# Kernel tuning notes

Measured on AMD Instinct MI355X. Metric: run time of the kernel, lower is better.

## Reference

```python
import jax, jax.numpy as jnp
import numpy as np

SCALE = 2
PAD = 4
EPS = 1e-5
K = 5
N, C, H, W = 4, 64, 128, 128


def _splits(a, s):
    # (..., W, H) -> (..., W/s, H/s, s*s), block decimation matching torch view/permute
    *lead, Wd, Hd = a.shape
    b = a.reshape(*lead, s, Wd // s, s, Hd // s)
    nl = len(lead)
    b = jnp.transpose(b, tuple(range(nl)) + (nl + 1, nl + 3, nl, nl + 2))
    return b.reshape(*lead, Wd // s, Hd // s, s * s)


def _p2o(psf, Hs, Ws):
    # PSF -> OTF: zero-pad, roll to center at origin, FFT
    kh, kw = psf.shape[-2], psf.shape[-1]
    otf = jnp.zeros(psf.shape[:-2] + (Hs, Ws), psf.dtype).at[..., :kh, :kw].set(psf)
    otf = jnp.roll(otf, (-(kh // 2), -(kw // 2)), axis=(-2, -1))
    return jnp.fft.fftn(otf, axes=(-2, -1))


def _upsample(x, s):
    # s-fold zero-filling upsampler (S^T y)
    n, c, h, w = x.shape
    return jnp.zeros((n, c, h * s, w * s), x.dtype).at[..., ::s, ::s].set(x)


def setup_inputs() -> dict:
    key = jax.random.key(0)
    kx, kw_, _ = jax.random.split(key, 3)
    x = jax.random.normal(kx, (N, C, H, W), dtype=jnp.float32)
    w_raw = jax.random.normal(kw_, (1, C, K, K), dtype=jnp.float32)
    weight = jax.nn.softmax(w_raw.reshape(1, C, -1), axis=-1).reshape(1, C, K, K)
    bias = jnp.zeros((1, C, 1, 1), dtype=jnp.float32)
    return {"x": x, "weight": weight, "bias": bias}


def reference(x, weight, bias):
    s = SCALE
    xp = jnp.pad(x, ((0, 0), (0, 0), (PAD, PAD), (PAD, PAD)), mode="wrap")  # circular
    biaseps = jax.nn.sigmoid(bias - 9.0) + EPS  # (1,C,1,1)
    _, _, h, w = xp.shape
    STy = _upsample(xp, s)  # zero-filled upsample
    # nearest-neighbor interpolate by integer factor s
    xn = jnp.repeat(jnp.repeat(xp, s, axis=-2), s, axis=-1)
    FB = _p2o(weight, h * s, w * s)           # (1,C,hs,ws) complex
    FBC = jnp.conj(FB)
    F2B = jnp.abs(FB) ** 2                     # real
    FBFy = FBC * jnp.fft.fftn(STy, axes=(-2, -1))
    FR = FBFy + jnp.fft.fftn(biaseps * xn, axes=(-2, -1))
    x1 = FB * FR
    FBR = jnp.mean(_splits(x1, s), axis=-1)    # (N,C,h,w) complex
    invW = jnp.mean(_splits(F2B, s), axis=-1)  # (1,C,h,w) real
    invWBR = FBR / (invW + biaseps)
    FCBinvWBR = FBC * jnp.tile(invWBR, (1, 1, s, s))
    FX = (FR - FCBinvWBR) / biaseps
    out = jnp.real(jnp.fft.ifftn(FX, axes=(-2, -1)))
    out = out[..., PAD * s:-PAD * s, PAD * s:-PAD * s]
    return out
```

## Files before the change

### kernel.cpp

```cpp
#include <hip/hip_runtime.h>
#include <math.h>


#define MDIM 136
#define RSC  70
#define HC   69
#define PLANE_HALF (MDIM*HC)
#define NPLANES 256
#define LDS_CPLX (MDIM*RSC + MDIM)
#define PI_D 3.14159265358979323846
#define NTH 1024

__device__ __forceinline__ int slot136(int k) { return 17*(k & 7) + (k >> 3); }
__device__ __forceinline__ int slot68(int k)  { return 17*(k & 3) + (k >> 2); }

template<int DIR, class F>
__device__ __forceinline__ void dft17_sink(float2* z, int base, int stride, F f)
{
    constexpr float C17[9] = {1.f, 0.93247223f, 0.73900892f, 0.44573836f,
                              0.09226836f, -0.27366299f, -0.60263464f,
                              -0.85021714f, -0.98297310f};
    constexpr float S17[9] = {0.f, 0.36124167f, 0.67369564f, 0.89516329f,
                              0.99573418f, 0.96182564f, 0.79801723f,
                              0.52643216f, 0.18374952f};
    constexpr float d = (DIR > 0) ? 1.f : -1.f;
    float xr[17], xi[17];
#pragma unroll
    for (int n = 0; n < 17; n++) {
        float2 v = z[base + n*stride];
        xr[n] = v.x; xi[n] = v.y;
    }
    float ar[8], ai[8], br[8], bi[8];
#pragma unroll
    for (int n = 1; n <= 8; n++) {
        ar[n-1] = xr[n] + xr[17-n];  ai[n-1] = xi[n] + xi[17-n];
        br[n-1] = xr[n] - xr[17-n];  bi[n-1] = xi[n] - xi[17-n];
    }
    float s0r = xr[0], s0i = xi[0];
#pragma unroll
    for (int n = 0; n < 8; n++) { s0r += ar[n]; s0i += ai[n]; }
    f(0, s0r, s0i);
#pragma unroll
    for (int k = 1; k <= 8; k++) {
        float Pr = xr[0], Pi = xi[0], Qr = 0.f, Qi = 0.f;
#pragma unroll
        for (int n = 1; n <= 8; n++) {
            int m = (k*n) % 17;
            float cc = (m <= 8) ? C17[m] : C17[17-m];
            float ss = (m <= 8) ? S17[m] : -S17[17-m];
            Pr = fmaf(ar[n-1], cc, Pr);
            Pi = fmaf(ai[n-1], cc, Pi);
            Qr = fmaf(br[n-1], ss, Qr);
            Qi = fmaf(bi[n-1], ss, Qi);
        }
        f(k,    Pr - d*Qi, Pi + d*Qr);
        f(17-k, Pr + d*Qi, Pi - d*Qr);
    }
}

template<int DIR>
__device__ __forceinline__ void radix4_tw(float2* z, const float2* lut, int base, int n2,
                                          float2 Z0, float2 Z1, float2 Z2, float2 Z3)
{
    constexpr float d = (DIR > 0) ? 1.0f : -1.0f;
    float t0r = Z0.x+Z2.x, t0i = Z0.y+Z2.y;
    float t1r = Z0.x-Z2.x, t1i = Z0.y-Z2.y;
    float t2r = Z1.x+Z3.x, t2i = Z1.y+Z3.y;
    float t3r = Z1.x-Z3.x, t3i = Z1.y-Z3.y;
    float X0r = t0r+t2r,     X0i = t0i+t2i;
    float X2r = t0r-t2r,     X2i = t0i-t2i;
    float X1r = t1r - d*t3i, X1i = t1i + d*t3r;
    float X3r = t1r + d*t3i, X3i = t1i - d*t3r;
    z[base + n2] = make_float2(X0r, X0i);
    float2 w1 = lut[2*n2], w2 = lut[4*n2], w3 = lut[6*n2];
    z[base + 17 + n2] = make_float2(X1r*w1.x - X1i*w1.y, X1r*w1.y + X1i*w1.x);
    z[base + 34 + n2] = make_float2(X2r*w2.x - X2i*w2.y, X2r*w2.y + X2i*w2.x);
    z[base + 51 + n2] = make_float2(X3r*w3.x - X3i*w3.y, X3r*w3.y + X3i*w3.x);
}

template<int DIR>
__device__ void fft136_s1(float2* z, const float2* lut, int ncols, int tid)
{
    constexpr float d = (DIR > 0) ? 1.0f : -1.0f;
    constexpr float C707 = 0.70710678118654752f;
    int c = tid / 17;
    int n2 = tid - c*17;
    for (int e = tid; e < ncols*17; e += NTH) {
        float xr[8], xi[8];
#pragma unroll
        for (int n1 = 0; n1 < 8; n1++) {
            float2 v = z[(17*n1 + n2)*RSC + c];
            xr[n1] = v.x; xi[n1] = v.y;
        }
        float e0r = xr[0]+xr[4], e0i = xi[0]+xi[4];
        float e1r = xr[0]-xr[4], e1i = xi[0]-xi[4];
        float o0r = xr[2]+xr[6], o0i = xi[2]+xi[6];
        float o1r = xr[2]-xr[6], o1i = xi[2]-xi[6];
        float E0r = e0r+o0r, E0i = e0i+o0i;
        float E2r = e0r-o0r, E2i = e0i-o0i;
        float E1r = e1r - d*o1i, E1i = e1i + d*o1r;
        float E3r = e1r + d*o1i, E3i = e1i - d*o1r;
        float f0r = xr[1]+xr[5], f0i = xi[1]+xi[5];
        float f1r = xr[1]-xr[5], f1i = xi[1]-xi[5];
        float h0r = xr[3]+xr[7], h0i = xi[3]+xi[7];
        float h1r = xr[3]-xr[7], h1i = xi[3]-xi[7];
        float O0r = f0r+h0r, O0i = f0i+h0i;
        float O2r = f0r-h0r, O2i = f0i-h0i;
        float O1r = f1r - d*h1i, O1i = f1i + d*h1r;
        float O3r = f1r + d*h1i, O3i = f1i - d*h1r;
        float t1r =  C707*(O1r - d*O1i), t1i = C707*(O1i + d*O1r);
        float t2r = -d*O2i,              t2i = d*O2r;
        float t3r = -C707*(O3r + d*O3i), t3i = C707*(d*O3r - O3i);
        float Xr[8], Xi[8];
        Xr[0]=E0r+O0r; Xi[0]=E0i+O0i;  Xr[4]=E0r-O0r; Xi[4]=E0i-O0i;
        Xr[1]=E1r+t1r; Xi[1]=E1i+t1i;  Xr[5]=E1r-t1r; Xi[5]=E1i-t1i;
        Xr[2]=E2r+t2r; Xi[2]=E2i+t2i;  Xr[6]=E2r-t2r; Xi[6]=E2i-t2i;
        Xr[3]=E3r+t3r; Xi[3]=E3i+t3i;  Xr[7]=E3r-t3r; Xi[7]=E3i-t3i;
        z[n2*RSC + c] = make_float2(Xr[0], Xi[0]);
        int ti = 0;
#pragma unroll
        for (int k1 = 1; k1 < 8; k1++) {
            ti += n2;
            float2 w = lut[ti];
            z[(17*k1 + n2)*RSC + c] = make_float2(Xr[k1]*w.x - Xi[k1]*w.y,
                                                  Xr[k1]*w.y + Xi[k1]*w.x);
        }
        c += 60; n2 += 4; if (n2 >= 17) { n2 -= 17; c++; }
    }
}

template<int DIR>
__device__ void ct68_s1(float2* z, const float2* lut, int tid)
{
    int row = tid / 17;
    int n2  = tid - row*17;
    for (int e = tid; e < MDIM*17; e += NTH) {
        int base = row*RSC;
        float2 Z0 = z[base + n2];
        float2 Z1 = z[base + 17 + n2];
        float2 Z2 = z[base + 34 + n2];
        float2 Z3 = z[base + 51 + n2];
        radix4_tw<DIR>(z, lut, base, n2, Z0, Z1, Z2, Z3);
        row += 60; n2 += 4; if (n2 >= 17) { n2 -= 17; row++; }
    }
}

__device__ __forceinline__ float2 c2r_pack(float2 a, float2 b, float2 w)
{
    float Sr = a.x + b.x, Si = a.y - b.y;
    float Dr = a.x - b.x, Di = a.y + b.y;
    float Or = w.x*Dr - w.y*Di, Oi = w.x*Di + w.y*Dr;
    return make_float2(Sr - Oi, Si + Or);
}

__global__ __launch_bounds__(1024, 8) void fwd_kernel(const float* __restrict__ x,
                                                      float2* __restrict__ Xhat)
{
    extern __shared__ float2 zsm[];
    float2* z   = zsm;
    float2* lut = zsm + MDIM*RSC;
    const int tid = threadIdx.x;

    if (tid < MDIM) {
        float s, c; sincosf(-2.0f*(float)PI_D*(float)tid/136.0f, &s, &c);
        lut[tid] = make_float2(c, s);
    }
    const float* xp = x + (size_t)blockIdx.x * (128*128);
    {
        int i = tid / 68, n = tid - (tid/68)*68;
        for (int e = tid; e < MDIM*68; e += NTH) {
            int si = (i + 124) & 127;
            int j0 = (2*n + 124) & 127;
            z[i*RSC + n] = *reinterpret_cast<const float2*>(xp + si*128 + j0);
            i += 15; n += 4; if (n >= 68) { n -= 68; i++; }
        }
    }
    __syncthreads();
    ct68_s1<-1>(z, lut, tid);
    __syncthreads();
    if (tid < MDIM*4) {
        int row = tid >> 2, k1 = tid & 3;
        int base = row*RSC + 17*k1;
        dft17_sink<-1>(z, base, 1, [&](int k2, float re, float im) {
            z[base + k2] = make_float2(re, im);
        });
    }
    __syncthreads();
    {
        int row = tid / 35, k = tid - (tid/35)*35;
        for (int e = tid; e < MDIM*35; e += NTH) {
            int base = row*RSC;
            int sa = slot68(k);
            float2 Za = z[base+sa];
            float Zar = Za.x, Zai = Za.y;
            float Zbr, Zbi; int sb;
            if (k == 0) { Zbr = Zar; Zbi = Zai; sb = 68; }
            else {
                int kk = 68-k; sb = slot68(kk);
                float2 Zb = z[base+sb]; Zbr = Zb.x; Zbi = Zb.y;
            }
            float2 w = lut[k];
            float wc = w.x, ws = w.y;
            float Er = 0.5f*(Zar + Zbr), Ei = 0.5f*(Zai - Zbi);
            float Dr = 0.5f*(Zar - Zbr), Di = 0.5f*(Zai + Zbi);
            float Tr = wc*Dr - ws*Di, Ti = wc*Di + ws*Dr;
            z[base+sa] = make_float2(Er + Ti, Ei - Tr);
            float E2r = Er,  E2i = -Ei;
            float D2r = -Dr, D2i = Di;
            float w2c = -wc, w2s = ws;
            float T2r = w2c*D2r - w2s*D2i, T2i = w2c*D2i + w2s*D2r;
            z[base+sb] = make_float2(E2r + T2i, E2i - T2r);
            row += 29; k += 9; if (k >= 35) { k -= 35; row++; }
        }
    }
    __syncthreads();
    fft136_s1<-1>(z, lut, HC, tid);
    __syncthreads();
    if (tid < HC*8) {
        int c = tid >> 3, k1 = tid & 7;
        int base = 17*k1*RSC + c;
        dft17_sink<-1>(z, base, RSC, [&](int k2, float re, float im) {
            z[base + k2*RSC] = make_float2(re, im);
        });
    }
    __syncthreads();
    float2* outp = Xhat + (size_t)blockIdx.x * PLANE_HALF;
    {
        int g1 = tid / HC, g2 = tid - (tid/HC)*HC;
        for (int e = tid; e < PLANE_HALF; e += NTH) {
            int cq = (g2 == 68) ? 68 : slot68(g2);
            outp[e] = z[slot136(g1)*RSC + cq];
            g1 += 14; g2 += 58; if (g2 >= HC) { g2 -= HC; g1++; }
        }
    }
}

__global__ void prep_kernel(const float* __restrict__ weight,
                            const float* __restrict__ bias,
                            float2* __restrict__ Abuf)
{
    __shared__ double tabc[272], tabs[272];
    for (int t = threadIdx.x; t < 272; t += blockDim.x) {
        double s, c; sincos(-2.0*PI_D*(double)t/272.0, &s, &c);
        tabc[t] = c; tabs[t] = s;
    }
    __syncthreads();

    const int c     = blockIdx.x >> 3;
    const int chunk = blockIdx.x & 7;
    const float* wp = weight + c*25;
    double w[25];
#pragma unroll
    for (int i = 0; i < 25; i++) w[i] = (double)wp[i];
    const double r = 1.0/(1.0 + exp(9.0 - (double)bias[c])) + 1e-5;

    const int e_lo = chunk * 1173;
    const int e_hi = e_lo + 1173;
    for (int e = e_lo + (int)threadIdx.x; e < e_hi; e += blockDim.x) {
        int g1 = e / HC, g2 = e - g1*HC;
        double c1 = tabc[g1], s1 = tabs[g1];
        double c2 = tabc[g2], s2 = tabs[g2];
        double e1r[5], e1i[5], e2r[5], e2i[5];
        e1r[2]=1.0; e1i[2]=0.0; e1r[3]=c1; e1i[3]=s1;
        e1r[4]=c1*c1-s1*s1; e1i[4]=2.0*c1*s1;
        e1r[1]=c1; e1i[1]=-s1; e1r[0]=e1r[4]; e1i[0]=-e1i[4];
        e2r[2]=1.0; e2i[2]=0.0; e2r[3]=c2; e2i[3]=s2;
        e2r[4]=c2*c2-s2*s2; e2i[4]=2.0*c2*s2;
        e2r[1]=c2; e2i[1]=-s2; e2r[0]=e2r[4]; e2i[0]=-e2i[4];

        double R0r[5],R0i[5],R1r[5],R1i[5];
#pragma unroll
        for (int a = 0; a < 5; a++) {
            double r0r=0,r0i=0,r1r=0,r1i=0;
#pragma unroll
            for (int b = 0; b < 5; b++) {
                double wv = w[a*5+b];
                double pr = wv*e2r[b], pi = wv*e2i[b];
                r0r += pr; r0i += pi;
                if (b & 1) { r1r -= pr; r1i -= pi; } else { r1r += pr; r1i += pi; }
            }
            R0r[a]=r0r; R0i[a]=r0i; R1r[a]=r1r; R1i[a]=r1i;
        }
        double FBr[2][2], FBi[2][2];
#pragma unroll
        for (int a1 = 0; a1 < 2; a1++)
#pragma unroll
            for (int b1 = 0; b1 < 2; b1++) {
                double fr=0, fi=0;
#pragma unroll
                for (int a = 0; a < 5; a++) {
                    double er = e1r[a], ei = e1i[a];
                    if (a1 && (a & 1)) { er = -er; ei = -ei; }
                    double Rr = b1 ? R1r[a] : R0r[a];
                    double Ri = b1 ? R1i[a] : R0i[a];
                    fr += er*Rr - ei*Ri;
                    fi += er*Ri + ei*Rr;
                }
                FBr[a1][b1]=fr; FBi[a1][b1]=fi;
            }
        double ur[2]={1.0+c1, 1.0-c1}, ui[2]={s1, -s1};
        double vr[2]={1.0+c2, 1.0-c2}, vi[2]={s2, -s2};
        double Br_[2][2], Bi_[2][2];
#pragma unroll
        for (int a1 = 0; a1 < 2; a1++)
#pragma unroll
            for (int b1 = 0; b1 < 2; b1++) {
                Br_[a1][b1] = ur[a1]*vr[b1] - ui[a1]*vi[b1];
                Bi_[a1][b1] = ur[a1]*vi[b1] + ui[a1]*vr[b1];
            }
        double invW=0, Qr=0, Qi=0;
#pragma unroll
        for (int a1 = 0; a1 < 2; a1++)
#pragma unroll
            for (int b1 = 0; b1 < 2; b1++) {
                invW += FBr[a1][b1]*FBr[a1][b1] + FBi[a1][b1]*FBi[a1][b1];
                Qr += FBr[a1][b1]*Br_[a1][b1] - FBi[a1][b1]*Bi_[a1][b1];
                Qi += FBr[a1][b1]*Bi_[a1][b1] + FBi[a1][b1]*Br_[a1][b1];
            }
        invW *= 0.25; Qr *= 0.25; Qi *= 0.25;
        double den = 1.0/(invW + r);
        double Sr = (1.0 - Qr)*den, Si = -Qi*den;
        double Mr[2][2], Mi[2][2];
#pragma unroll
        for (int a1 = 0; a1 < 2; a1++)
#pragma unroll
            for (int b1 = 0; b1 < 2; b1++) {
                Mr[a1][b1] = Br_[a1][b1] + FBr[a1][b1]*Sr + FBi[a1][b1]*Si;
                Mi[a1][b1] = Bi_[a1][b1] + FBr[a1][b1]*Si - FBi[a1][b1]*Sr;
            }
        const double scale = 1.0/73984.0;
#pragma unroll
        for (int uu = 0; uu < 2; uu++)
#pragma unroll
            for (int vv = 0; vv < 2; vv++) {
                double sr=0, si=0;
#pragma unroll
                for (int a1 = 0; a1 < 2; a1++)
#pragma unroll
                    for (int b1 = 0; b1 < 2; b1++) {
                        if ((a1*uu + b1*vv) & 1) { sr -= Mr[a1][b1]; si -= Mi[a1][b1]; }
                        else                     { sr += Mr[a1][b1]; si += Mi[a1][b1]; }
                    }
                int t = g1*uu + g2*vv;
                double pc = tabc[t], ps = -tabs[t];
                float2 outv;
                outv.x = (float)((pc*sr - ps*si)*scale);
                outv.y = (float)((pc*si + ps*sr)*scale);
                Abuf[((size_t)(c*4 + uu*2 + vv))*PLANE_HALF + e] = outv;
            }
    }
}

__global__ __launch_bounds__(1024, 8) void inv_kernel(const float2* __restrict__ Xhat,
                                                      const float2* __restrict__ Abuf,
                                                      float* __restrict__ out)
{
    extern __shared__ float2 zsm[];
    float2* z   = zsm;
    float2* lut = zsm + MDIM*RSC;
    const int tid = threadIdx.x;

    if (tid < MDIM) {
        float s, c; sincosf(2.0f*(float)PI_D*(float)tid/136.0f, &s, &c);
        lut[tid] = make_float2(c, s);
    }
    const int p  = blockIdx.x;
    const int u  = p & 1;
    const int v  = (p >> 3) & 1;
    const int nc = ((p >> 4) << 2) | ((p >> 1) & 3);
    const int c  = nc & 63;
    const float2* Xp = Xhat + (size_t)nc * PLANE_HALF;
    const float2* Ap = Abuf + (size_t)(c*4 + u*2 + v) * PLANE_HALF;

    {
        int g1 = tid / HC, g2 = tid - (tid/HC)*HC;
        for (int e = tid; e < PLANE_HALF; e += NTH) {
            float2 xv = Xp[e], av = Ap[e];
            z[g1*RSC + g2] = make_float2(av.x*xv.x - av.y*xv.y,
                                         av.x*xv.y + av.y*xv.x);
            g1 += 14; g2 += 58; if (g2 >= HC) { g2 -= HC; g1++; }
        }
    }
    __syncthreads();
    fft136_s1<1>(z, lut, HC, tid);
    __syncthreads();
    if (tid < HC*8) {
        int cc = tid >> 3, k1 = tid & 7;
        int base = 17*k1*RSC + cc;
        dft17_sink<1>(z, base, RSC, [&](int k2, float re, float im) {
            z[base + k2*RSC] = make_float2(re, im);
        });
    }
    __syncthreads();
    {
        int row = tid / 9, g = tid - (tid/9)*9;
        for (int e = tid; e < MDIM*9; e += NTH) {
            int base = row*RSC;
            if (g == 0) {
                float2 T0  = z[base],    T17 = z[base+17], T34 = z[base+34],
                       T51 = z[base+51], T68 = z[base+68];
                float2 Z0 = c2r_pack(T0,  T68, lut[0]);
                float2 Z1 = c2r_pack(T17, T51, lut[17]);
                float2 Z2 = c2r_pack(T34, T34, lut[34]);
                float2 Z3 = c2r_pack(T51, T17, lut[51]);
                radix4_tw<1>(z, lut, base, 0, Z0, Z1, Z2, Z3);
            } else {
                int gb = 17 - g;
                float2 Ta0 = z[base+g],    Ta1 = z[base+g+17],
                       Ta2 = z[base+g+34], Ta3 = z[base+g+51];
                float2 Tb0 = z[base+gb],    Tb1 = z[base+gb+17],
                       Tb2 = z[base+gb+34], Tb3 = z[base+gb+51];
                float2 Za0 = c2r_pack(Ta0, Tb3, lut[g]);
                float2 Za1 = c2r_pack(Ta1, Tb2, lut[g+17]);
                float2 Za2 = c2r_pack(Ta2, Tb1, lut[g+34]);
                float2 Za3 = c2r_pack(Ta3, Tb0, lut[g+51]);
                float2 Zb0 = c2r_pack(Tb0, Ta3, lut[gb]);
                float2 Zb1 = c2r_pack(Tb1, Ta2, lut[gb+17]);
                float2 Zb2 = c2r_pack(Tb2, Ta1, lut[gb+34]);
                float2 Zb3 = c2r_pack(Tb3, Ta0, lut[gb+51]);
                radix4_tw<1>(z, lut, base, g,  Za0, Za1, Za2, Za3);
                radix4_tw<1>(z, lut, base, gb, Zb0, Zb1, Zb2, Zb3);
            }
            row += 113; g += 7; if (g >= 9) { g -= 9; row++; }
        }
    }
    __syncthreads();
    if (tid < MDIM*4) {
        int row = tid >> 2, k1 = tid & 3;
        int base = row*RSC + 17*k1;
        dft17_sink<1>(z, base, 1, [&](int k2, float re, float im) {
            z[base + k2] = make_float2(re, im);
        });
    }
    __syncthreads();
    float* op = out + (size_t)nc * (256*256);
    {
        int m  = 2 + (tid & 63);
        int y1 = 4 + (tid >> 6);
        int a  = slot136(y1)*RSC + slot68(m);
        float* rowp = op + (size_t)(2*y1 + u - 8)*256 + 4*m + v - 8;
#pragma unroll
        for (int it = 0; it < 8; ++it) {
            float2 wv = z[a];
            rowp[0] = wv.x;
            rowp[2] = wv.y;
            a += 2*RSC;
            rowp += 32*256;
        }
    }
}

extern "C" void kernel_launch(void* const* d_in, const int* in_sizes, int n_in,
                              void* d_out, int out_size, void* d_ws, size_t ws_size,
                              hipStream_t stream)
{
    const float* x      = (const float*)d_in[0];
    const float* weight = (const float*)d_in[1];
    const float* bias   = (const float*)d_in[2];
    float* out = (float*)d_out;

    float2* Xhat = (float2*)d_ws;
    float2* Abuf = Xhat + (size_t)NPLANES * PLANE_HALF;

    const size_t lds_bytes = (size_t)LDS_CPLX * sizeof(float2);
    (void)hipFuncSetAttribute((const void*)fwd_kernel,
                              hipFuncAttributeMaxDynamicSharedMemorySize, (int)lds_bytes);
    (void)hipFuncSetAttribute((const void*)inv_kernel,
                              hipFuncAttributeMaxDynamicSharedMemorySize, (int)lds_bytes);

    prep_kernel<<<512, 256, 0, stream>>>(weight, bias, Abuf);
    fwd_kernel<<<NPLANES, 1024, lds_bytes, stream>>>(x, Xhat);
    inv_kernel<<<NPLANES*4, 1024, lds_bytes, stream>>>(Xhat, Abuf, out);
}
```

Measured before the change: 150.3 us.

## Process two v-phase planes per inverse block to share Xhat loads

Each inverse-FFT block now handles both v-phase sub-planes of an output plane, keeping two LDS buffers. The block reads the Xhat spectrum once for both, runs the FFT stages over both planes in flattened loops, and writes interleaved outputs with float4 stores. The grid is halved. In exchange LDS per block roughly doubles, which lowers the number of resident blocks per CU, and the launch bound is reduced accordingly.

New measurement: 144.9 us. -3.5%, faster.

```diff
diff --git a/kernel.cpp b/kernel.cpp
--- a/kernel.cpp
+++ b/kernel.cpp
@@ -7,7 +7,8 @@
 #define HC   69
 #define PLANE_HALF (MDIM*HC)
 #define NPLANES 256
-#define LDS_CPLX (MDIM*RSC + MDIM)
+#define LDS_CPLX  (MDIM*RSC + MDIM)
+#define LDS_CPLX2 (2*MDIM*RSC + MDIM)
 #define PI_D 3.14159265358979323846
 #define NTH 1024
 
@@ -79,52 +80,59 @@
 }
 
 template<int DIR>
-__device__ void fft136_s1(float2* z, const float2* lut, int ncols, int tid)
+__device__ __forceinline__ void fft136_s1_body(float2* z, const float2* lut,
+                                               int c, int n2)
 {
     constexpr float d = (DIR > 0) ? 1.0f : -1.0f;
     constexpr float C707 = 0.70710678118654752f;
+    float xr[8], xi[8];
+#pragma unroll
+    for (int n1 = 0; n1 < 8; n1++) {
+        float2 v = z[(17*n1 + n2)*RSC + c];
+        xr[n1] = v.x; xi[n1] = v.y;
+    }
+    float e0r = xr[0]+xr[4], e0i = xi[0]+xi[4];
+    float e1r = xr[0]-xr[4], e1i = xi[0]-xi[4];
+    float o0r = xr[2]+xr[6], o0i = xi[2]+xi[6];
+    float o1r = xr[2]-xr[6], o1i = xi[2]-xi[6];
+    float E0r = e0r+o0r, E0i = e0i+o0i;
+    float E2r = e0r-o0r, E2i = e0i-o0i;
+    float E1r = e1r - d*o1i, E1i = e1i + d*o1r;
+    float E3r = e1r + d*o1i, E3i = e1i - d*o1r;
+    float f0r = xr[1]+xr[5], f0i = xi[1]+xi[5];
+    float f1r = xr[1]-xr[5], f1i = xi[1]-xi[5];
+    float h0r = xr[3]+xr[7], h0i = xi[3]+xi[7];
+    float h1r = xr[3]-xr[7], h1i = xi[3]-xi[7];
+    float O0r = f0r+h0r, O0i = f0i+h0i;
+    float O2r = f0r-h0r, O2i = f0i-h0i;
+    float O1r = f1r - d*h1i, O1i = f1i + d*h1r;
+    float O3r = f1r + d*h1i, O3i = f1i - d*h1r;
+    float t1r =  C707*(O1r - d*O1i), t1i = C707*(O1i + d*O1r);
+    float t2r = -d*O2i,              t2i = d*O2r;
+    float t3r = -C707*(O3r + d*O3i), t3i = C707*(d*O3r - O3i);
+    float Xr[8], Xi[8];
+    Xr[0]=E0r+O0r; Xi[0]=E0i+O0i;  Xr[4]=E0r-O0r; Xi[4]=E0i-O0i;
+    Xr[1]=E1r+t1r; Xi[1]=E1i+t1i;  Xr[5]=E1r-t1r; Xi[5]=E1i-t1i;
+    Xr[2]=E2r+t2r; Xi[2]=E2i+t2i;  Xr[6]=E2r-t2r; Xi[6]=E2i-t2i;
+    Xr[3]=E3r+t3r; Xi[3]=E3i+t3i;  Xr[7]=E3r-t3r; Xi[7]=E3i-t3i;
+    z[n2*RSC + c] = make_float2(Xr[0], Xi[0]);
+    int ti = 0;
+#pragma unroll
+    for (int k1 = 1; k1 < 8; k1++) {
+        ti += n2;
+        float2 w = lut[ti];
+        z[(17*k1 + n2)*RSC + c] = make_float2(Xr[k1]*w.x - Xi[k1]*w.y,
+                                              Xr[k1]*w.y + Xi[k1]*w.x);
+    }
+}
+
+template<int DIR>
+__device__ void fft136_s1(float2* z, const float2* lut, int ncols, int tid)
+{
     int c = tid / 17;
     int n2 = tid - c*17;
     for (int e = tid; e < ncols*17; e += NTH) {
-        float xr[8], xi[8];
-#pragma unroll
-        for (int n1 = 0; n1 < 8; n1++) {
-            float2 v = z[(17*n1 + n2)*RSC + c];
-            xr[n1] = v.x; xi[n1] = v.y;
-        }
-        float e0r = xr[0]+xr[4], e0i = xi[0]+xi[4];
-        float e1r = xr[0]-xr[4], e1i = xi[0]-xi[4];
-        float o0r = xr[2]+xr[6], o0i = xi[2]+xi[6];
-        float o1r = xr[2]-xr[6], o1i = xi[2]-xi[6];
-        float E0r = e0r+o0r, E0i = e0i+o0i;
-        float E2r = e0r-o0r, E2i = e0i-o0i;
-        float E1r = e1r - d*o1i, E1i = e1i + d*o1r;
-        float E3r = e1r + d*o1i, E3i = e1i - d*o1r;
-        float f0r = xr[1]+xr[5], f0i = xi[1]+xi[5];
-        float f1r = xr[1]-xr[5], f1i = xi[1]-xi[5];
-        float h0r = xr[3]+xr[7], h0i = xi[3]+xi[7];
-        float h1r = xr[3]-xr[7], h1i = xi[3]-xi[7];
-        float O0r = f0r+h0r, O0i = f0i+h0i;
-        float O2r = f0r-h0r, O2i = f0i-h0i;
-        float O1r = f1r - d*h1i, O1i = f1i + d*h1r;
-        float O3r = f1r + d*h1i, O3i = f1i - d*h1r;
-        float t1r =  C707*(O1r - d*O1i), t1i = C707*(O1i + d*O1r);
-        float t2r = -d*O2i,              t2i = d*O2r;
-        float t3r = -C707*(O3r + d*O3i), t3i = C707*(d*O3r - O3i);
-        float Xr[8], Xi[8];
-        Xr[0]=E0r+O0r; Xi[0]=E0i+O0i;  Xr[4]=E0r-O0r; Xi[4]=E0i-O0i;
-        Xr[1]=E1r+t1r; Xi[1]=E1i+t1i;  Xr[5]=E1r-t1r; Xi[5]=E1i-t1i;
-        Xr[2]=E2r+t2r; Xi[2]=E2i+t2i;  Xr[6]=E2r-t2r; Xi[6]=E2i-t2i;
-        Xr[3]=E3r+t3r; Xi[3]=E3i+t3i;  Xr[7]=E3r-t3r; Xi[7]=E3i-t3i;
-        z[n2*RSC + c] = make_float2(Xr[0], Xi[0]);
-        int ti = 0;
-#pragma unroll
-        for (int k1 = 1; k1 < 8; k1++) {
-            ti += n2;
-            float2 w = lut[ti];
-            z[(17*k1 + n2)*RSC + c] = make_float2(Xr[k1]*w.x - Xi[k1]*w.y,
-                                                  Xr[k1]*w.y + Xi[k1]*w.x);
-        }
+        fft136_s1_body<DIR>(z, lut, c, n2);
         c += 60; n2 += 4; if (n2 >= 17) { n2 -= 17; c++; }
     }
 }
@@ -351,13 +359,14 @@
     }
 }
 
-__global__ __launch_bounds__(1024, 8) void inv_kernel(const float2* __restrict__ Xhat,
+__global__ __launch_bounds__(1024, 4) void inv_kernel(const float2* __restrict__ Xhat,
                                                       const float2* __restrict__ Abuf,
                                                       float* __restrict__ out)
 {
     extern __shared__ float2 zsm[];
-    float2* z   = zsm;
-    float2* lut = zsm + MDIM*RSC;
+    float2* z0  = zsm;
+    float2* z1  = zsm + MDIM*RSC;
+    float2* lut = zsm + 2*MDIM*RSC;
     const int tid = threadIdx.x;
 
     if (tid < MDIM) {
@@ -365,71 +374,85 @@
         lut[tid] = make_float2(c, s);
     }
     const int p  = blockIdx.x;
-    const int u  = p & 1;
-    const int v  = (p >> 3) & 1;
-    const int nc = ((p >> 4) << 2) | ((p >> 1) & 3);
+    const int u  = (p >> 3) & 1;
+    const int nc = ((p >> 4) << 3) | (p & 7);
     const int c  = nc & 63;
-    const float2* Xp = Xhat + (size_t)nc * PLANE_HALF;
-    const float2* Ap = Abuf + (size_t)(c*4 + u*2 + v) * PLANE_HALF;
+    const float2* Xp  = Xhat + (size_t)nc * PLANE_HALF;
+    const float2* Ap0 = Abuf + (size_t)(c*4 + u*2) * PLANE_HALF;
+    const float2* Ap1 = Ap0 + PLANE_HALF;
 
     {
         int g1 = tid / HC, g2 = tid - (tid/HC)*HC;
         for (int e = tid; e < PLANE_HALF; e += NTH) {
-            float2 xv = Xp[e], av = Ap[e];
-            z[g1*RSC + g2] = make_float2(av.x*xv.x - av.y*xv.y,
-                                         av.x*xv.y + av.y*xv.x);
+            float2 xv = Xp[e], a0 = Ap0[e], a1 = Ap1[e];
+            int a = g1*RSC + g2;
+            z0[a] = make_float2(a0.x*xv.x - a0.y*xv.y, a0.x*xv.y + a0.y*xv.x);
+            z1[a] = make_float2(a1.x*xv.x - a1.y*xv.y, a1.x*xv.y + a1.y*xv.x);
             g1 += 14; g2 += 58; if (g2 >= HC) { g2 -= HC; g1++; }
         }
     }
     __syncthreads();
-    fft136_s1<1>(z, lut, HC, tid);
-    __syncthreads();
-    if (tid < HC*8) {
-        int cc = tid >> 3, k1 = tid & 7;
+    for (int it = tid; it < 2*HC*17; it += NTH) {
+        int pl = it >= HC*17;
+        int ee = it - (pl ? HC*17 : 0);
+        int cc = (ee*241) >> 12;
+        int n2 = ee - cc*17;
+        fft136_s1_body<1>(pl ? z1 : z0, lut, cc, n2);
+    }
+    __syncthreads();
+    for (int it = tid; it < 2*HC*8; it += NTH) {
+        int pl = it >= HC*8;
+        int i  = it - (pl ? HC*8 : 0);
+        float2* zz = pl ? z1 : z0;
+        int cc = i >> 3, k1 = i & 7;
         int base = 17*k1*RSC + cc;
-        dft17_sink<1>(z, base, RSC, [&](int k2, float re, float im) {
-            z[base + k2*RSC] = make_float2(re, im);
+        dft17_sink<1>(zz, base, RSC, [&](int k2, float re, float im) {
+            zz[base + k2*RSC] = make_float2(re, im);
         });
     }
     __syncthreads();
-    {
-        int row = tid / 9, g = tid - (tid/9)*9;
-        for (int e = tid; e < MDIM*9; e += NTH) {
-            int base = row*RSC;
-            if (g == 0) {
-                float2 T0  = z[base],    T17 = z[base+17], T34 = z[base+34],
-                       T51 = z[base+51], T68 = z[base+68];
-                float2 Z0 = c2r_pack(T0,  T68, lut[0]);
-                float2 Z1 = c2r_pack(T17, T51, lut[17]);
-                float2 Z2 = c2r_pack(T34, T34, lut[34]);
-                float2 Z3 = c2r_pack(T51, T17, lut[51]);
-                radix4_tw<1>(z, lut, base, 0, Z0, Z1, Z2, Z3);
-            } else {
-                int gb = 17 - g;
-                float2 Ta0 = z[base+g],    Ta1 = z[base+g+17],
-                       Ta2 = z[base+g+34], Ta3 = z[base+g+51];
-                float2 Tb0 = z[base+gb],    Tb1 = z[base+gb+17],
-                       Tb2 = z[base+gb+34], Tb3 = z[base+gb+51];
-                float2 Za0 = c2r_pack(Ta0, Tb3, lut[g]);
-                float2 Za1 = c2r_pack(Ta1, Tb2, lut[g+17]);
-                float2 Za2 = c2r_pack(Ta2, Tb1, lut[g+34]);
-                float2 Za3 = c2r_pack(Ta3, Tb0, lut[g+51]);
-                float2 Zb0 = c2r_pack(Tb0, Ta3, lut[gb]);
-                float2 Zb1 = c2r_pack(Tb1, Ta2, lut[gb+17]);
-                float2 Zb2 = c2r_pack(Tb2, Ta1, lut[gb+34]);
-                float2 Zb3 = c2r_pack(Tb3, Ta0, lut[gb+51]);
-                radix4_tw<1>(z, lut, base, g,  Za0, Za1, Za2, Za3);
-                radix4_tw<1>(z, lut, base, gb, Zb0, Zb1, Zb2, Zb3);
-            }
-            row += 113; g += 7; if (g >= 9) { g -= 9; row++; }
-        }
-    }
-    __syncthreads();
-    if (tid < MDIM*4) {
-        int row = tid >> 2, k1 = tid & 3;
+    for (int it = tid; it < 2*MDIM*9; it += NTH) {
+        int pl = it >= MDIM*9;
+        int i  = it - (pl ? MDIM*9 : 0);
+        float2* zz = pl ? z1 : z0;
+        int row = (i*7282) >> 16;
+        int g   = i - row*9;
+        int base = row*RSC;
+        if (g == 0) {
+            float2 T0  = zz[base],    T17 = zz[base+17], T34 = zz[base+34],
+                   T51 = zz[base+51], T68 = zz[base+68];
+            float2 Z0 = c2r_pack(T0,  T68, lut[0]);
+            float2 Z1 = c2r_pack(T17, T51, lut[17]);
+            float2 Z2 = c2r_pack(T34, T34, lut[34]);
+            float2 Z3 = c2r_pack(T51, T17, lut[51]);
+            radix4_tw<1>(zz, lut, base, 0, Z0, Z1, Z2, Z3);
+        } else {
+            int gb = 17 - g;
+            float2 Ta0 = zz[base+g],    Ta1 = zz[base+g+17],
+                   Ta2 = zz[base+g+34], Ta3 = zz[base+g+51];
+            float2 Tb0 = zz[base+gb],    Tb1 = zz[base+gb+17],
+                   Tb2 = zz[base+gb+34], Tb3 = zz[base+gb+51];
+            float2 Za0 = c2r_pack(Ta0, Tb3, lut[g]);
+            float2 Za1 = c2r_pack(Ta1, Tb2, lut[g+17]);
+            float2 Za2 = c2r_pack(Ta2, Tb1, lut[g+34]);
+            float2 Za3 = c2r_pack(Ta3, Tb0, lut[g+51]);
+            float2 Zb0 = c2r_pack(Tb0, Ta3, lut[gb]);
+            float2 Zb1 = c2r_pack(Tb1, Ta2, lut[gb+17]);
+            float2 Zb2 = c2r_pack(Tb2, Ta1, lut[gb+34]);
+            float2 Zb3 = c2r_pack(Tb3, Ta0, lut[gb+51]);
+            radix4_tw<1>(zz, lut, base, g,  Za0, Za1, Za2, Za3);
+            radix4_tw<1>(zz, lut, base, gb, Zb0, Zb1, Zb2, Zb3);
+        }
+    }
+    __syncthreads();
+    for (int it = tid; it < 2*MDIM*4; it += NTH) {
+        int pl = it >= MDIM*4;
+        int i  = it - (pl ? MDIM*4 : 0);
+        float2* zz = pl ? z1 : z0;
+        int row = i >> 2, k1 = i & 3;
         int base = row*RSC + 17*k1;
-        dft17_sink<1>(z, base, 1, [&](int k2, float re, float im) {
-            z[base + k2] = make_float2(re, im);
+        dft17_sink<1>(zz, base, 1, [&](int k2, float re, float im) {
+            zz[base + k2] = make_float2(re, im);
         });
     }
     __syncthreads();
@@ -438,12 +461,11 @@
         int m  = 2 + (tid & 63);
         int y1 = 4 + (tid >> 6);
         int a  = slot136(y1)*RSC + slot68(m);
-        float* rowp = op + (size_t)(2*y1 + u - 8)*256 + 4*m + v - 8;
+        float* rowp = op + (size_t)(2*y1 + u - 8)*256 + 4*m - 8;
 #pragma unroll
         for (int it = 0; it < 8; ++it) {
-            float2 wv = z[a];
-            rowp[0] = wv.x;
-            rowp[2] = wv.y;
+            float2 w0 = z0[a], w1 = z1[a];
+            *reinterpret_cast<float4*>(rowp) = make_float4(w0.x, w1.x, w0.y, w1.y);
             a += 2*RSC;
             rowp += 32*256;
         }
@@ -462,13 +484,14 @@
     float2* Xhat = (float2*)d_ws;
     float2* Abuf = Xhat + (size_t)NPLANES * PLANE_HALF;
 
-    const size_t lds_bytes = (size_t)LDS_CPLX * sizeof(float2);
+    const size_t lds_fwd = (size_t)LDS_CPLX  * sizeof(float2);
+    const size_t lds_inv = (size_t)LDS_CPLX2 * sizeof(float2);
     (void)hipFuncSetAttribute((const void*)fwd_kernel,
-                              hipFuncAttributeMaxDynamicSharedMemorySize, (int)lds_bytes);
+                              hipFuncAttributeMaxDynamicSharedMemorySize, (int)lds_fwd);
     (void)hipFuncSetAttribute((const void*)inv_kernel,
-                              hipFuncAttributeMaxDynamicSharedMemorySize, (int)lds_bytes);
+                              hipFuncAttributeMaxDynamicSharedMemorySize, (int)lds_inv);
 
     prep_kernel<<<512, 256, 0, stream>>>(weight, bias, Abuf);
-    fwd_kernel<<<NPLANES, 1024, lds_bytes, stream>>>(x, Xhat);
-    inv_kernel<<<NPLANES*4, 1024, lds_bytes, stream>>>(Xhat, Abuf, out);
-}
+    fwd_kernel<<<NPLANES, 1024, lds_fwd, stream>>>(x, Xhat);
+    inv_kernel<<<NPLANES*2, 1024, lds_inv, stream>>>(Xhat, Abuf, out);
+}
```
